# Performance work log

Hardware: AMD Instinct MI355X
Metric: run time of the kernel (lower is better)

Reference implementation:

```python
import jax, jax.numpy as jnp
import numpy as np

N, E, D = 50000, 800000, 128
CLAMP = 2.0  # coord_weights_clamp_value


def setup_inputs() -> dict:
    key = jax.random.key(0)
    ks = jax.random.split(key, 12)
    rn = lambda k, shape, scale: jax.random.normal(k, shape, jnp.float32) * scale
    s = lambda fan_in: 1.0 / np.sqrt(fan_in)
    h = rn(ks[0], (N, D), 1.0)
    x = rn(ks[1], (N, 3), 1.0)
    edges = jax.random.randint(ks[2], (2, E), 0, N)
    # edge MLP: Linear(2D+1 -> D), SiLU, Linear(D -> D), SiLU
    we1 = rn(ks[3], (2 * D + 1, D), s(2 * D + 1)); be1 = jnp.zeros((D,), jnp.float32)
    we2 = rn(ks[4], (D, D), s(D));                 be2 = jnp.zeros((D,), jnp.float32)
    # node MLP: Linear(2D -> D), SiLU, Linear(D -> D)
    wn1 = rn(ks[5], (2 * D, D), s(2 * D));         bn1 = jnp.zeros((D,), jnp.float32)
    wn2 = rn(ks[6], (D, D), s(D));                 bn2 = jnp.zeros((D,), jnp.float32)
    # coord MLP: Linear(D -> D), SiLU, Linear(D -> 1, no bias, small init)
    wc1 = rn(ks[7], (D, D), s(D));                 bc1 = jnp.zeros((D,), jnp.float32)
    wc2 = rn(ks[8], (D, 1), 0.001)
    return dict(h=h, x=x, edges=edges, we1=we1, be1=be1, we2=we2, be2=be2,
                wn1=wn1, bn1=bn1, wn2=wn2, bn2=bn2, wc1=wc1, bc1=bc1, wc2=wc2)


def reference(h, x, edges, we1, be1, we2, be2, wn1, bn1, wn2, bn2, wc1, bc1, wc2):
    n = h.shape[0]
    row, col = edges[0], edges[1]
    # coord2radial
    coord_diff = x[row] - x[col]                                  # [E, 3]
    radial = jnp.sum(coord_diff * coord_diff, axis=1, keepdims=True)  # [E, 1]
    # edge model: phi_e(h_i, h_j, ||x_i - x_j||^2)
    e_in = jnp.concatenate([h[row], h[col], radial], axis=1)      # [E, 2D+1]
    m = jax.nn.silu(jax.nn.silu(e_in @ we1 + be1) @ we2 + be2)    # [E, D]
    # coord model: x_i += mean_j (x_i - x_j) * phi_x(m_ij), clamped
    w = jax.nn.silu(m @ wc1 + bc1) @ wc2                          # [E, 1]
    trans = jnp.clip(coord_diff * w, -CLAMP, CLAMP)               # [E, 3]
    ones = jnp.ones((row.shape[0], 1), m.dtype)
    cnt = jax.ops.segment_sum(ones, row, num_segments=n)          # [N, 1]
    agg_x = jax.ops.segment_sum(trans, row, num_segments=n) / jnp.maximum(cnt, 1.0)
    x_out = x + agg_x
    # node model: h_i += phi_h(h_i, sum_j m_ij)  (residual=True)
    agg_m = jax.ops.segment_sum(m, row, num_segments=n)           # [N, D]
    h_up = jax.nn.silu(jnp.concatenate([h, agg_m], axis=1) @ wn1 + bn1) @ wn2 + bn2
    h_out = h + h_up
    return (h_out, x_out)
```

## Files before the change

### kernel.cpp

```cpp
#include <hip/hip_runtime.h>
#include <hip/hip_bf16.h>
#include <stdint.h>

typedef unsigned short u16;
typedef __bf16 bf16x8 __attribute__((ext_vector_type(8)));
typedef float f32x4 __attribute__((ext_vector_type(4)));

#define DD 128

__device__ __forceinline__ u16 f2bf(float f) {
  uint32_t r;
  asm("v_cvt_pk_bf16_f32 %0, %1, %2" : "=v"(r) : "v"(f), "v"(f));
  return (u16)r;
}
__device__ __forceinline__ float bf2f(u16 h) {
  union { uint32_t u; float f; } v; v.u = ((uint32_t)h) << 16;
  return v.f;
}
__device__ __forceinline__ uint32_t pack2(float a, float b) {
  uint32_t r;
  asm("v_cvt_pk_bf16_f32 %0, %1, %2" : "=v"(r) : "v"(a), "v"(b));
  return r;
}
__device__ __forceinline__ float silu_(float v) {
  return v * __builtin_amdgcn_rcpf(1.0f + __expf(-v));
}
__device__ __forceinline__ f32x4 MFMA(bf16x8 a, bf16x8 b, f32x4 c) {
  return __builtin_amdgcn_mfma_f32_16x16x32_bf16(a, b, c, 0, 0, 0);
}
#define LGKM_FENCE() do { asm volatile("s_waitcnt lgkmcnt(0)" ::: "memory"); __builtin_amdgcn_sched_barrier(0); } while (0)

__global__ __launch_bounds__(256) void kprep(
    const float* __restrict__ we1, const float* __restrict__ we2,
    const float* __restrict__ wn1, const float* __restrict__ wn2,
    const float* __restrict__ wc1, u16* __restrict__ frags) {
  const int total = 16384 * 5 + 32768;
  for (int idx = blockIdx.x * blockDim.x + threadIdx.x; idx < total;
       idx += gridDim.x * blockDim.x) {
    const float* src; int segbase;
    if (idx < 16384)      { src = we1;          segbase = 0; }
    else if (idx < 32768) { src = we1 + 16384;  segbase = 16384; }
    else if (idx < 49152) { src = we2;          segbase = 32768; }
    else if (idx < 65536) { src = wc1;          segbase = 49152; }
    else if (idx < 81920) { src = wn2;          segbase = 65536; }
    else                  { src = wn1;          segbase = 81920; }
    int local = idx - segbase;
    int k = local >> 7, n = local & 127;
    float v = src[k * 128 + n];
    int s = k >> 5, i = k & 7, g = (k >> 3) & 3;
    int lane = (g << 4) | (n & 15), f = n >> 4;
    frags[segbase + (((s * 8 + f) * 64 + lane) << 3) + i] = f2bf(v);
  }
}

__global__ __launch_bounds__(256) void kpq(
    const float* __restrict__ h, const float* __restrict__ be1,
    const u16* __restrict__ wA, const u16* __restrict__ wB,
    u16* __restrict__ Pb, u16* __restrict__ Qb, int N) {
  __shared__ u16 act[64 * 128];
  const int tid = threadIdx.x;
  const int w = tid >> 6, l = tid & 63;
  const int lm = l & 15, lh = l >> 4;
  const int base = blockIdx.x * 64;

  {
    const int q = l & 3;
    const int rowL = w * 16 + (l >> 2);
    int node = base + rowL; if (node >= N) node = N - 1;
    const float* hs = h + (size_t)node * 128 + q * 32;
    #pragma unroll
    for (int c4 = 0; c4 < 4; ++c4) {
      float4 v0 = *(const float4*)(hs + c4 * 8);
      float4 v1 = *(const float4*)(hs + c4 * 8 + 4);
      uint4 pk;
      pk.x = pack2(v0.x, v0.y); pk.y = pack2(v0.z, v0.w);
      pk.z = pack2(v1.x, v1.y); pk.w = pack2(v1.z, v1.w);
      int c = q * 4 + c4;
      *(uint4*)&act[rowL * 128 + (((c ^ (rowL & 7))) << 3)] = pk;
    }
  }
  LGKM_FENCE();
  const int rowA = w * 16 + lm, sw = rowA & 7;
  bf16x8 a[4];
  #pragma unroll
  for (int s = 0; s < 4; ++s)
    a[s] = *(const bf16x8*)&act[rowA * 128 + (((4 * s + lh) ^ sw) << 3)];
  float be1r[8];
  #pragma unroll
  for (int f = 0; f < 8; ++f) be1r[f] = be1[16 * f + lm];

  f32x4 acc[8] = {};
  #pragma unroll
  for (int s = 0; s < 4; ++s)
    #pragma unroll
    for (int f = 0; f < 8; ++f)
      acc[f] = MFMA(a[s], *(const bf16x8*)(wA + (((s * 8 + f) * 64 + l) << 3)), acc[f]);
  #pragma unroll
  for (int f = 0; f < 8; ++f)
    #pragma unroll
    for (int r = 0; r < 4; ++r) {
      int row = base + w * 16 + lh * 4 + r;
      Pb[(size_t)row * 128 + 16 * f + lm] = f2bf(acc[f][r] + be1r[f]);
    }

  f32x4 acc2[8] = {};
  #pragma unroll
  for (int s = 0; s < 4; ++s)
    #pragma unroll
    for (int f = 0; f < 8; ++f)
      acc2[f] = MFMA(a[s], *(const bf16x8*)(wB + (((s * 8 + f) * 64 + l) << 3)), acc2[f]);
  #pragma unroll
  for (int f = 0; f < 8; ++f)
    #pragma unroll
    for (int r = 0; r < 4; ++r) {
      int row = base + w * 16 + lh * 4 + r;
      Qb[(size_t)row * 128 + 16 * f + lm] = f2bf(acc2[f][r]);
    }
}


__global__ __launch_bounds__(256) void kedgeA(
    const float* __restrict__ x, const int* __restrict__ edges,
    const float* __restrict__ we1, const float* __restrict__ be2,
    const float* __restrict__ bc1, const float* __restrict__ wc2,
    const u16* __restrict__ Pb, const u16* __restrict__ Qb,
    const u16* __restrict__ we2f, const u16* __restrict__ wc1f,
    u16* __restrict__ mT, float* __restrict__ trans4, int E) {
  __shared__ u16 act[64 * 128];
  __shared__ float w1c[128];
  const int tid = threadIdx.x;
  if (tid < 128) w1c[tid] = we1[256 * 128 + tid];
  __syncthreads();

  const int w = tid >> 6, l = tid & 63;
  const int lm = l & 15, lh = l >> 4;
  float be2r[8], bc1r[8], wc2r[8];
  #pragma unroll
  for (int f = 0; f < 8; ++f) {
    be2r[f] = be2[16 * f + lm];
    bc1r[f] = bc1[16 * f + lm];
    wc2r[f] = wc2[16 * f + lm];
  }

  const int tb = blockIdx.x * 64 + w * 16;
  int eMine = tb + lm;
  int eC = eMine < E ? eMine : E - 1;
  const int rowv = edges[eC];
  const int colv = edges[E + eC];
  float cdx = x[rowv * 3]     - x[colv * 3];
  float cdy = x[rowv * 3 + 1] - x[colv * 3 + 1];
  float cdz = x[rowv * 3 + 2] - x[colv * 3 + 2];
  float radial = cdx * cdx + cdy * cdy + cdz * cdz;

  {
    const int el = l >> 2, q = l & 3;
    int rG = __shfl(rowv, el), cG = __shfl(colv, el);
    float rad = __shfl(radial, el);
    const int rowL = w * 16 + el;
    const u16* Pp = Pb + (size_t)rG * 128 + q * 32;
    const u16* Qp = Qb + (size_t)cG * 128 + q * 32;
    #pragma unroll
    for (int c4 = 0; c4 < 4; ++c4) {
      uint4 pv = *(const uint4*)(Pp + c4 * 8);
      uint4 qv = *(const uint4*)(Qp + c4 * 8);
      uint32_t pw[4] = {pv.x, pv.y, pv.z, pv.w};
      uint32_t qw[4] = {qv.x, qv.y, qv.z, qv.w};
      uint32_t ow[4];
      #pragma unroll
      for (int jj = 0; jj < 4; ++jj) {
        int fb = q * 32 + c4 * 8 + jj * 2;
        float t0 = bf2f((u16)(pw[jj] & 0xffff)) + bf2f((u16)(qw[jj] & 0xffff)) + rad * w1c[fb];
        float t1 = bf2f((u16)(pw[jj] >> 16))    + bf2f((u16)(qw[jj] >> 16))    + rad * w1c[fb + 1];
        ow[jj] = pack2(silu_(t0), silu_(t1));
      }
      int c = q * 4 + c4;
      *(uint4*)&act[rowL * 128 + ((c ^ (rowL & 7)) << 3)] =
          make_uint4(ow[0], ow[1], ow[2], ow[3]);
    }
  }
  LGKM_FENCE();

  const int rowA = w * 16 + lm, sw = rowA & 7;
  bf16x8 a[4];
  #pragma unroll
  for (int s = 0; s < 4; ++s)
    a[s] = *(const bf16x8*)&act[rowA * 128 + (((4 * s + lh) ^ sw) << 3)];

  f32x4 acc[8] = {};
  #pragma unroll
  for (int s = 0; s < 4; ++s)
    #pragma unroll
    for (int f = 0; f < 8; ++f)
      acc[f] = MFMA(a[s], *(const bf16x8*)(we2f + (((s * 8 + f) * 64 + l) << 3)), acc[f]);

  bool ev[4];
  #pragma unroll
  for (int r = 0; r < 4; ++r) ev[r] = (tb + lh * 4 + r) < E;
  u16* mTb = mT + (size_t)(blockIdx.x * 4 + w) * 2048;

  #pragma unroll
  for (int f = 0; f < 8; ++f)
    #pragma unroll
    for (int r = 0; r < 4; ++r) {
      float m = silu_(acc[f][r] + be2r[f]);
      u16 mv = f2bf(m);
      int row = w * 16 + lh * 4 + r, col = 16 * f + lm;
      act[row * 128 + (((col >> 3) ^ (row & 7)) << 3) + (col & 7)] = mv;
      if (ev[r]) mTb[((lh * 4 + r) * 16 + lm) * 8 + f] = mv;
    }
  LGKM_FENCE();

  bf16x8 a2[4];
  #pragma unroll
  for (int s = 0; s < 4; ++s)
    a2[s] = *(const bf16x8*)&act[rowA * 128 + (((4 * s + lh) ^ sw) << 3)];
  f32x4 acc3[8] = {};
  #pragma unroll
  for (int s = 0; s < 4; ++s)
    #pragma unroll
    for (int f = 0; f < 8; ++f)
      acc3[f] = MFMA(a2[s], *(const bf16x8*)(wc1f + (((s * 8 + f) * 64 + l) << 3)), acc3[f]);

  float wp[4] = {0.f, 0.f, 0.f, 0.f};
  #pragma unroll
  for (int f = 0; f < 8; ++f)
    #pragma unroll
    for (int r = 0; r < 4; ++r)
      wp[r] += silu_(acc3[f][r] + bc1r[f]) * wc2r[f];
  #pragma unroll
  for (int r = 0; r < 4; ++r) {
    wp[r] += __shfl_xor(wp[r], 1);
    wp[r] += __shfl_xor(wp[r], 2);
    wp[r] += __shfl_xor(wp[r], 4);
    wp[r] += __shfl_xor(wp[r], 8);
  }
  #pragma unroll
  for (int r = 0; r < 4; ++r) {
    int erv = __shfl(rowv, lh * 4 + r);
    float cdxr = __shfl(cdx, lh * 4 + r);
    float cdyr = __shfl(cdy, lh * 4 + r);
    float cdzr = __shfl(cdz, lh * 4 + r);
    if (lm < 4 && ev[r]) {
      float wv = wp[r];
      float v3;
      if (lm == 0)      v3 = fminf(fmaxf(cdxr * wv, -2.0f), 2.0f);
      else if (lm == 1) v3 = fminf(fmaxf(cdyr * wv, -2.0f), 2.0f);
      else if (lm == 2) v3 = fminf(fmaxf(cdzr * wv, -2.0f), 2.0f);
      else              v3 = __int_as_float(erv);
      trans4[(size_t)(tb + lh * 4 + r) * 4 + lm] = v3;
    }
  }
}

__global__ __launch_bounds__(256) void kscat(
    const u16* __restrict__ mT, const float* __restrict__ trans4,
    float* __restrict__ aggm, float* __restrict__ aggx, int E) {
  const int tid = threadIdx.x;
  const int w = tid >> 6, l = tid & 63;
  const int lh = l >> 4, lm = l & 15;
  const int tile = blockIdx.x * 4 + w;
  const int tb = tile * 16;

  const u16* base = mT + (size_t)tile * 2048;
  bf16x8 ch[4];
  #pragma unroll
  for (int r = 0; r < 4; ++r)
    ch[r] = *(const bf16x8*)(base + ((lh * 4 + r) * 16 + lm) * 8);

  int eL = tb + (l >> 2);
  float tv = (eL < E) ? trans4[(size_t)eL * 4 + (l & 3)] : __int_as_float(-1);

  int erOwn = __float_as_int(__shfl(tv, (l >> 2) * 4 + 3));
  if (erOwn >= 0) {
    float val = ((l & 3) == 3) ? 1.0f : tv;
    unsafeAtomicAdd(&aggx[(size_t)erOwn * 4 + (l & 3)], val);
  }

  #pragma unroll
  for (int r = 0; r < 4; ++r) {
    int er = __float_as_int(__shfl(tv, (lh * 4 + r) * 4 + 3));
    if (er >= 0) {
      const u16* hp = (const u16*)&ch[r];
      #pragma unroll
      for (int f = 0; f < 8; ++f)
        unsafeAtomicAdd(&aggm[(size_t)er * 128 + 16 * f + lm], bf2f(hp[f]));
    }
  }
}

__global__ __launch_bounds__(256) void kedge_mono(
    const float* __restrict__ x, const int* __restrict__ edges,
    const float* __restrict__ we1, const float* __restrict__ be2,
    const float* __restrict__ bc1, const float* __restrict__ wc2,
    const u16* __restrict__ Pb, const u16* __restrict__ Qb,
    const u16* __restrict__ we2f, const u16* __restrict__ wc1f,
    float* __restrict__ aggm, float* __restrict__ aggx, int E) {
  __shared__ u16 act[64 * 128];
  __shared__ float w1c[128];
  const int tid = threadIdx.x;
  if (tid < 128) w1c[tid] = we1[256 * 128 + tid];
  __syncthreads();

  const int w = tid >> 6, l = tid & 63;
  const int lm = l & 15, lh = l >> 4;
  float be2r[8], bc1r[8], wc2r[8];
  #pragma unroll
  for (int f = 0; f < 8; ++f) {
    be2r[f] = be2[16 * f + lm];
    bc1r[f] = bc1[16 * f + lm];
    wc2r[f] = wc2[16 * f + lm];
  }

  const int tb = blockIdx.x * 64 + w * 16;
  int eMine = tb + lm;
  int eC = eMine < E ? eMine : E - 1;
  const int rowv = edges[eC];
  const int colv = edges[E + eC];
  float cdx = x[rowv * 3]     - x[colv * 3];
  float cdy = x[rowv * 3 + 1] - x[colv * 3 + 1];
  float cdz = x[rowv * 3 + 2] - x[colv * 3 + 2];
  float radial = cdx * cdx + cdy * cdy + cdz * cdz;

  {
    const int el = l >> 2, q = l & 3;
    int rG = __shfl(rowv, el), cG = __shfl(colv, el);
    float rad = __shfl(radial, el);
    const int rowL = w * 16 + el;
    const u16* Pp = Pb + (size_t)rG * 128 + q * 32;
    const u16* Qp = Qb + (size_t)cG * 128 + q * 32;
    #pragma unroll
    for (int c4 = 0; c4 < 4; ++c4) {
      uint4 pv = *(const uint4*)(Pp + c4 * 8);
      uint4 qv = *(const uint4*)(Qp + c4 * 8);
      uint32_t pw[4] = {pv.x, pv.y, pv.z, pv.w};
      uint32_t qw[4] = {qv.x, qv.y, qv.z, qv.w};
      uint32_t ow[4];
      #pragma unroll
      for (int jj = 0; jj < 4; ++jj) {
        int fb = q * 32 + c4 * 8 + jj * 2;
        float t0 = bf2f((u16)(pw[jj] & 0xffff)) + bf2f((u16)(qw[jj] & 0xffff)) + rad * w1c[fb];
        float t1 = bf2f((u16)(pw[jj] >> 16))    + bf2f((u16)(qw[jj] >> 16))    + rad * w1c[fb + 1];
        ow[jj] = pack2(silu_(t0), silu_(t1));
      }
      int c = q * 4 + c4;
      *(uint4*)&act[rowL * 128 + ((c ^ (rowL & 7)) << 3)] =
          make_uint4(ow[0], ow[1], ow[2], ow[3]);
    }
  }
  LGKM_FENCE();

  const int rowA = w * 16 + lm, sw = rowA & 7;
  bf16x8 a[4];
  #pragma unroll
  for (int s = 0; s < 4; ++s)
    a[s] = *(const bf16x8*)&act[rowA * 128 + (((4 * s + lh) ^ sw) << 3)];

  f32x4 acc[8] = {};
  #pragma unroll
  for (int s = 0; s < 4; ++s)
    #pragma unroll
    for (int f = 0; f < 8; ++f)
      acc[f] = MFMA(a[s], *(const bf16x8*)(we2f + (((s * 8 + f) * 64 + l) << 3)), acc[f]);

  #pragma unroll
  for (int f = 0; f < 8; ++f)
    #pragma unroll
    for (int r = 0; r < 4; ++r) {
      float m = silu_(acc[f][r] + be2r[f]);
      int row = w * 16 + lh * 4 + r, col = 16 * f + lm;
      act[row * 128 + (((col >> 3) ^ (row & 7)) << 3) + (col & 7)] = f2bf(m);
    }
  LGKM_FENCE();

  bf16x8 a2[4];
  #pragma unroll
  for (int s = 0; s < 4; ++s)
    a2[s] = *(const bf16x8*)&act[rowA * 128 + (((4 * s + lh) ^ sw) << 3)];
  f32x4 acc3[8] = {};
  #pragma unroll
  for (int s = 0; s < 4; ++s)
    #pragma unroll
    for (int f = 0; f < 8; ++f)
      acc3[f] = MFMA(a2[s], *(const bf16x8*)(wc1f + (((s * 8 + f) * 64 + l) << 3)), acc3[f]);

  float wp[4] = {0.f, 0.f, 0.f, 0.f};
  #pragma unroll
  for (int f = 0; f < 8; ++f)
    #pragma unroll
    for (int r = 0; r < 4; ++r)
      wp[r] += silu_(acc3[f][r] + bc1r[f]) * wc2r[f];
  #pragma unroll
  for (int r = 0; r < 4; ++r) {
    wp[r] += __shfl_xor(wp[r], 1);
    wp[r] += __shfl_xor(wp[r], 2);
    wp[r] += __shfl_xor(wp[r], 4);
    wp[r] += __shfl_xor(wp[r], 8);
  }
  int er[4]; bool vr[4];
  float cdxr[4], cdyr[4], cdzr[4];
  #pragma unroll
  for (int r = 0; r < 4; ++r) {
    er[r] = __shfl(rowv, lh * 4 + r);
    vr[r] = (tb + lh * 4 + r) < E;
    cdxr[r] = __shfl(cdx, lh * 4 + r);
    cdyr[r] = __shfl(cdy, lh * 4 + r);
    cdzr[r] = __shfl(cdz, lh * 4 + r);
  }

  if (lm < 4) {
    #pragma unroll
    for (int r = 0; r < 4; ++r) {
      if (vr[r]) {
        float wv = wp[r];
        float v3;
        if (lm == 0)      v3 = fminf(fmaxf(cdxr[r] * wv, -2.0f), 2.0f);
        else if (lm == 1) v3 = fminf(fmaxf(cdyr[r] * wv, -2.0f), 2.0f);
        else if (lm == 2) v3 = fminf(fmaxf(cdzr[r] * wv, -2.0f), 2.0f);
        else              v3 = 1.0f;
        unsafeAtomicAdd(&aggx[(size_t)er[r] * 4 + lm], v3);
      }
    }
  }
  #pragma unroll
  for (int f = 0; f < 8; ++f)
    #pragma unroll
    for (int r = 0; r < 4; ++r) {
      if (vr[r]) {
        float m = silu_(acc[f][r] + be2r[f]);
        unsafeAtomicAdd(&aggm[(size_t)er[r] * 128 + 16 * f + lm], m);
      }
    }
}

__global__ __launch_bounds__(256) void knode(
    const float* __restrict__ h, const float* __restrict__ x,
    const float* __restrict__ aggm, const float* __restrict__ aggx,
    const float* __restrict__ bn1, const float* __restrict__ bn2,
    const u16* __restrict__ wn1f, const u16* __restrict__ wn2f,
    float* __restrict__ out, int N) {
  __shared__ u16 act[64 * 256];
  __shared__ u16 act2[64 * 128];
  const int tid = threadIdx.x;
  const int w = tid >> 6, l = tid & 63;
  const int lm = l & 15, lh = l >> 4;
  const int base = blockIdx.x * 64;

  if (tid < 192) {
    int n = base + tid / 3, c = tid - (tid / 3) * 3;
    if (n < N) {
      float ct = fmaxf(aggx[(size_t)n * 4 + 3], 1.0f);
      out[(size_t)N * 128 + (size_t)n * 3 + c] =
          x[(size_t)n * 3 + c] + aggx[(size_t)n * 4 + c] / ct;
    }
  }

  {
    const int q = l & 3;
    const int rowL = w * 16 + (l >> 2);
    int node = base + rowL; if (node >= N) node = N - 1;
    const float* src = (q < 2) ? (h + (size_t)node * 128 + q * 64)
                               : (aggm + (size_t)node * 128 + (q - 2) * 64);
    #pragma unroll
    for (int c8 = 0; c8 < 8; ++c8) {
      float4 v0 = *(const float4*)(src + c8 * 8);
      float4 v1 = *(const float4*)(src + c8 * 8 + 4);
      uint4 pk;
      pk.x = pack2(v0.x, v0.y); pk.y = pack2(v0.z, v0.w);
      pk.z = pack2(v1.x, v1.y); pk.w = pack2(v1.z, v1.w);
      int c = q * 8 + c8;
      *(uint4*)&act[rowL * 256 + ((c ^ (rowL & 7)) << 3)] = pk;
    }
  }
  LGKM_FENCE();

  const int rowA = w * 16 + lm, sw = rowA & 7;
  float bn1r[8], bn2r[8];
  #pragma unroll
  for (int f = 0; f < 8; ++f) {
    bn1r[f] = bn1[16 * f + lm];
    bn2r[f] = bn2[16 * f + lm];
  }
  bf16x8 a[8];
  #pragma unroll
  for (int s = 0; s < 8; ++s)
    a[s] = *(const bf16x8*)&act[rowA * 256 + (((4 * s + lh) ^ sw) << 3)];
  f32x4 acc[8] = {};
  #pragma unroll
  for (int s = 0; s < 8; ++s)
    #pragma unroll
    for (int f = 0; f < 8; ++f)
      acc[f] = MFMA(a[s], *(const bf16x8*)(wn1f + (((s * 8 + f) * 64 + l) << 3)), acc[f]);
  #pragma unroll
  for (int f = 0; f < 8; ++f)
    #pragma unroll
    for (int r = 0; r < 4; ++r) {
      int row = w * 16 + lh * 4 + r, col = 16 * f + lm;
      act2[row * 128 + (((col >> 3) ^ (row & 7)) << 3) + (col & 7)] =
          f2bf(silu_(acc[f][r] + bn1r[f]));
    }
  LGKM_FENCE();

  bf16x8 a2[4];
  #pragma unroll
  for (int s = 0; s < 4; ++s)
    a2[s] = *(const bf16x8*)&act2[rowA * 128 + (((4 * s + lh) ^ sw) << 3)];
  f32x4 acc2[8] = {};
  #pragma unroll
  for (int s = 0; s < 4; ++s)
    #pragma unroll
    for (int f = 0; f < 8; ++f)
      acc2[f] = MFMA(a2[s], *(const bf16x8*)(wn2f + (((s * 8 + f) * 64 + l) << 3)), acc2[f]);
  #pragma unroll
  for (int f = 0; f < 8; ++f)
    #pragma unroll
    for (int r = 0; r < 4; ++r) {
      int n2 = base + w * 16 + lh * 4 + r;
      if (n2 < N) {
        int col = 16 * f + lm;
        out[(size_t)n2 * 128 + col] =
            h[(size_t)n2 * 128 + col] + acc2[f][r] + bn2r[f];
      }
    }
}

extern "C" void kernel_launch(void* const* d_in, const int* in_sizes, int n_in,
                              void* d_out, int out_size, void* d_ws, size_t ws_size,
                              hipStream_t stream) {
  const float* h   = (const float*)d_in[0];
  const float* x   = (const float*)d_in[1];
  const int* edges = (const int*)d_in[2];
  const float* we1 = (const float*)d_in[3];
  const float* be1 = (const float*)d_in[4];
  const float* we2 = (const float*)d_in[5];
  const float* be2 = (const float*)d_in[6];
  const float* wn1 = (const float*)d_in[7];
  const float* bn1 = (const float*)d_in[8];
  const float* wn2 = (const float*)d_in[9];
  const float* bn2 = (const float*)d_in[10];
  const float* wc1 = (const float*)d_in[11];
  const float* bc1 = (const float*)d_in[12];
  const float* wc2 = (const float*)d_in[13];

  const int N = in_sizes[0] / DD;
  const int E = in_sizes[2] / 2;
  const int NT = (N + 63) & ~63;
  const int ET = (E + 15) & ~15;

  u16* Pb    = (u16*)d_ws;
  u16* Qb    = Pb + (size_t)NT * DD;
  u16* frags = Qb + (size_t)NT * DD;
  float* aggm = (float*)(frags + 114688);
  float* aggx = aggm + (size_t)NT * DD;
  u16* mT     = (u16*)(aggx + (size_t)NT * 4);
  float* trans4 = (float*)(mT + (size_t)ET * DD);

  size_t need_small = (size_t)NT * DD * 2 * 2 + 114688 * 2 +
                      (size_t)NT * (DD * 4 + 16);
  size_t need_big = need_small + (size_t)ET * DD * 2 + (size_t)ET * 16;
  if (ws_size < need_small) return;

  hipMemsetAsync(aggm, 0, (size_t)NT * (DD * 4 + 16), stream);
  hipLaunchKernelGGL(kprep, dim3(64), dim3(256), 0, stream,
                     we1, we2, wn1, wn2, wc1, frags);
  hipLaunchKernelGGL(kpq, dim3(NT / 64), dim3(256), 0, stream,
                     h, be1, frags, frags + 16384, Pb, Qb, N);
  if (ws_size >= need_big) {
    hipLaunchKernelGGL(kedgeA, dim3((E + 63) / 64), dim3(256), 0, stream,
                       x, edges, we1, be2, bc1, wc2, Pb, Qb,
                       frags + 32768, frags + 49152, mT, trans4, E);
    hipLaunchKernelGGL(kscat, dim3((ET / 16 + 3) / 4), dim3(256), 0, stream,
                       mT, trans4, aggm, aggx, E);
  } else {
    hipLaunchKernelGGL(kedge_mono, dim3((E + 63) / 64), dim3(256), 0, stream,
                       x, edges, we1, be2, bc1, wc2, Pb, Qb,
                       frags + 32768, frags + 49152, aggm, aggx, E);
  }
  hipLaunchKernelGGL(knode, dim3(NT / 64), dim3(256), 0, stream,
                     h, x, aggm, aggx, bn1, bn2,
                     frags + 81920, frags + 65536, (float*)d_out, N);
}
```

Baseline: 453.9 us.

## Fuse edge MLP with scatter atomics and prefetch next tile's P/Q gathers

Replaces the two-kernel edge path (edge MLP writing m and trans to a buffer, then a separate scatter kernel) with one kernel that does the atomics for agg_m and agg_x directly. Each wave now handles four 16-edge tiles and prefetches the next tile's P/Q rows while the current tile runs its MFMAs. Coordinate differences and radial are precomputed by a small kernel and stored as bf16. This removes the round trip of the m buffer through global memory but cuts coordinate precision to bf16, and it raises register pressure from the prefetch buffers.

```diff
diff --git a/kernel.cpp b/kernel.cpp
--- a/kernel.cpp
+++ b/kernel.cpp
@@ -5,6 +5,7 @@
 typedef unsigned short u16;
 typedef __bf16 bf16x8 __attribute__((ext_vector_type(8)));
 typedef float f32x4 __attribute__((ext_vector_type(4)));
+typedef unsigned int u32x4 __attribute__((ext_vector_type(4)));
 
 #define DD 128
 
@@ -53,6 +54,19 @@
   }
 }
 
+__global__ __launch_bounds__(256) void kradial(
+    const int* __restrict__ edges, const float* __restrict__ x,
+    uint2* __restrict__ cdr, int E) {
+  int i = blockIdx.x * 256 + threadIdx.x;
+  if (i >= E) return;
+  int r = edges[i], c = edges[E + i];
+  float dx = x[r * 3]     - x[c * 3];
+  float dy = x[r * 3 + 1] - x[c * 3 + 1];
+  float dz = x[r * 3 + 2] - x[c * 3 + 2];
+  float rad = dx * dx + dy * dy + dz * dz;
+  cdr[i] = make_uint2(pack2(dx, dy), pack2(dz, rad));
+}
+
 __global__ __launch_bounds__(256) void kpq(
     const float* __restrict__ h, const float* __restrict__ be1,
     const u16* __restrict__ wA, const u16* __restrict__ wB,
@@ -118,14 +132,13 @@
     }
 }
 
-
-__global__ __launch_bounds__(256) void kedgeA(
-    const float* __restrict__ x, const int* __restrict__ edges,
+__global__ __launch_bounds__(256) void kedgeP(
+    const int* __restrict__ edges, const uint2* __restrict__ cdr,
     const float* __restrict__ we1, const float* __restrict__ be2,
     const float* __restrict__ bc1, const float* __restrict__ wc2,
     const u16* __restrict__ Pb, const u16* __restrict__ Qb,
     const u16* __restrict__ we2f, const u16* __restrict__ wc1f,
-    u16* __restrict__ mT, float* __restrict__ trans4, int E) {
+    float* __restrict__ aggm, float* __restrict__ aggx, int E) {
   __shared__ u16 act[64 * 128];
   __shared__ float w1c[128];
   const int tid = threadIdx.x;
@@ -134,6 +147,7 @@
 
   const int w = tid >> 6, l = tid & 63;
   const int lm = l & 15, lh = l >> 4;
+  const int el = l >> 2, q = l & 3;
   float be2r[8], bc1r[8], wc2r[8];
   #pragma unroll
   for (int f = 0; f < 8; ++f) {
@@ -142,148 +156,161 @@
     wc2r[f] = wc2[16 * f + lm];
   }
 
-  const int tb = blockIdx.x * 64 + w * 16;
-  int eMine = tb + lm;
-  int eC = eMine < E ? eMine : E - 1;
-  const int rowv = edges[eC];
-  const int colv = edges[E + eC];
-  float cdx = x[rowv * 3]     - x[colv * 3];
-  float cdy = x[rowv * 3 + 1] - x[colv * 3 + 1];
-  float cdz = x[rowv * 3 + 2] - x[colv * 3 + 2];
-  float radial = cdx * cdx + cdy * cdy + cdz * cdz;
-
+  const int tb = blockIdx.x * 256 + w * 64;
+  const int rowA = w * 16 + lm, sw = rowA & 7;
+  const int rowL = w * 16 + el;
+
+  int rv[4], cv[4]; uint2 cdu[4];
+  #pragma unroll
+  for (int t = 0; t < 4; ++t) {
+    int e = tb + t * 16 + lm;
+    int ec = e < E ? e : E - 1;
+    rv[t] = edges[ec];
+    cv[t] = edges[E + ec];
+    cdu[t] = cdr[ec];
+  }
+
+  u32x4 Pc[4], Qc[4], Pn[4], Qn[4];
   {
-    const int el = l >> 2, q = l & 3;
-    int rG = __shfl(rowv, el), cG = __shfl(colv, el);
-    float rad = __shfl(radial, el);
-    const int rowL = w * 16 + el;
+    int rG = __shfl(rv[0], el), cG = __shfl(cv[0], el);
     const u16* Pp = Pb + (size_t)rG * 128 + q * 32;
     const u16* Qp = Qb + (size_t)cG * 128 + q * 32;
     #pragma unroll
     for (int c4 = 0; c4 < 4; ++c4) {
-      uint4 pv = *(const uint4*)(Pp + c4 * 8);
-      uint4 qv = *(const uint4*)(Qp + c4 * 8);
-      uint32_t pw[4] = {pv.x, pv.y, pv.z, pv.w};
-      uint32_t qw[4] = {qv.x, qv.y, qv.z, qv.w};
-      uint32_t ow[4];
-      #pragma unroll
-      for (int jj = 0; jj < 4; ++jj) {
-        int fb = q * 32 + c4 * 8 + jj * 2;
-        float t0 = bf2f((u16)(pw[jj] & 0xffff)) + bf2f((u16)(qw[jj] & 0xffff)) + rad * w1c[fb];
-        float t1 = bf2f((u16)(pw[jj] >> 16))    + bf2f((u16)(qw[jj] >> 16))    + rad * w1c[fb + 1];
-        ow[jj] = pack2(silu_(t0), silu_(t1));
-      }
-      int c = q * 4 + c4;
-      *(uint4*)&act[rowL * 128 + ((c ^ (rowL & 7)) << 3)] =
-          make_uint4(ow[0], ow[1], ow[2], ow[3]);
-    }
-  }
-  LGKM_FENCE();
-
-  const int rowA = w * 16 + lm, sw = rowA & 7;
-  bf16x8 a[4];
-  #pragma unroll
-  for (int s = 0; s < 4; ++s)
-    a[s] = *(const bf16x8*)&act[rowA * 128 + (((4 * s + lh) ^ sw) << 3)];
-
-  f32x4 acc[8] = {};
-  #pragma unroll
-  for (int s = 0; s < 4; ++s)
-    #pragma unroll
-    for (int f = 0; f < 8; ++f)
-      acc[f] = MFMA(a[s], *(const bf16x8*)(we2f + (((s * 8 + f) * 64 + l) << 3)), acc[f]);
-
-  bool ev[4];
-  #pragma unroll
-  for (int r = 0; r < 4; ++r) ev[r] = (tb + lh * 4 + r) < E;
-  u16* mTb = mT + (size_t)(blockIdx.x * 4 + w) * 2048;
-
-  #pragma unroll
-  for (int f = 0; f < 8; ++f)
-    #pragma unroll
-    for (int r = 0; r < 4; ++r) {
-      float m = silu_(acc[f][r] + be2r[f]);
-      u16 mv = f2bf(m);
-      int row = w * 16 + lh * 4 + r, col = 16 * f + lm;
-      act[row * 128 + (((col >> 3) ^ (row & 7)) << 3) + (col & 7)] = mv;
-      if (ev[r]) mTb[((lh * 4 + r) * 16 + lm) * 8 + f] = mv;
-    }
-  LGKM_FENCE();
-
-  bf16x8 a2[4];
-  #pragma unroll
-  for (int s = 0; s < 4; ++s)
-    a2[s] = *(const bf16x8*)&act[rowA * 128 + (((4 * s + lh) ^ sw) << 3)];
-  f32x4 acc3[8] = {};
-  #pragma unroll
-  for (int s = 0; s < 4; ++s)
-    #pragma unroll
-    for (int f = 0; f < 8; ++f)
-      acc3[f] = MFMA(a2[s], *(const bf16x8*)(wc1f + (((s * 8 + f) * 64 + l) << 3)), acc3[f]);
-
-  float wp[4] = {0.f, 0.f, 0.f, 0.f};
-  #pragma unroll
-  for (int f = 0; f < 8; ++f)
-    #pragma unroll
-    for (int r = 0; r < 4; ++r)
-      wp[r] += silu_(acc3[f][r] + bc1r[f]) * wc2r[f];
-  #pragma unroll
-  for (int r = 0; r < 4; ++r) {
-    wp[r] += __shfl_xor(wp[r], 1);
-    wp[r] += __shfl_xor(wp[r], 2);
-    wp[r] += __shfl_xor(wp[r], 4);
-    wp[r] += __shfl_xor(wp[r], 8);
-  }
-  #pragma unroll
-  for (int r = 0; r < 4; ++r) {
-    int erv = __shfl(rowv, lh * 4 + r);
-    float cdxr = __shfl(cdx, lh * 4 + r);
-    float cdyr = __shfl(cdy, lh * 4 + r);
-    float cdzr = __shfl(cdz, lh * 4 + r);
-    if (lm < 4 && ev[r]) {
-      float wv = wp[r];
-      float v3;
-      if (lm == 0)      v3 = fminf(fmaxf(cdxr * wv, -2.0f), 2.0f);
-      else if (lm == 1) v3 = fminf(fmaxf(cdyr * wv, -2.0f), 2.0f);
-      else if (lm == 2) v3 = fminf(fmaxf(cdzr * wv, -2.0f), 2.0f);
-      else              v3 = __int_as_float(erv);
-      trans4[(size_t)(tb + lh * 4 + r) * 4 + lm] = v3;
-    }
-  }
-}
-
-__global__ __launch_bounds__(256) void kscat(
-    const u16* __restrict__ mT, const float* __restrict__ trans4,
-    float* __restrict__ aggm, float* __restrict__ aggx, int E) {
-  const int tid = threadIdx.x;
-  const int w = tid >> 6, l = tid & 63;
-  const int lh = l >> 4, lm = l & 15;
-  const int tile = blockIdx.x * 4 + w;
-  const int tb = tile * 16;
-
-  const u16* base = mT + (size_t)tile * 2048;
-  bf16x8 ch[4];
-  #pragma unroll
-  for (int r = 0; r < 4; ++r)
-    ch[r] = *(const bf16x8*)(base + ((lh * 4 + r) * 16 + lm) * 8);
-
-  int eL = tb + (l >> 2);
-  float tv = (eL < E) ? trans4[(size_t)eL * 4 + (l & 3)] : __int_as_float(-1);
-
-  int erOwn = __float_as_int(__shfl(tv, (l >> 2) * 4 + 3));
-  if (erOwn >= 0) {
-    float val = ((l & 3) == 3) ? 1.0f : tv;
-    unsafeAtomicAdd(&aggx[(size_t)erOwn * 4 + (l & 3)], val);
-  }
-
-  #pragma unroll
-  for (int r = 0; r < 4; ++r) {
-    int er = __float_as_int(__shfl(tv, (lh * 4 + r) * 4 + 3));
-    if (er >= 0) {
-      const u16* hp = (const u16*)&ch[r];
+      Pc[c4] = *(const u32x4*)(Pp + c4 * 8);
+      Qc[c4] = *(const u32x4*)(Qp + c4 * 8);
+    }
+  }
+
+  #pragma unroll
+  for (int t = 0; t < 4; ++t) {
+    {
+      float radf = bf2f((u16)(cdu[t].y >> 16));
+      float rad = __shfl(radf, el);
+      #pragma unroll
+      for (int c4 = 0; c4 < 4; ++c4) {
+        uint32_t pw[4] = {Pc[c4].x, Pc[c4].y, Pc[c4].z, Pc[c4].w};
+        uint32_t qw[4] = {Qc[c4].x, Qc[c4].y, Qc[c4].z, Qc[c4].w};
+        uint32_t ow[4];
+        #pragma unroll
+        for (int jj = 0; jj < 4; ++jj) {
+          int fb = q * 32 + c4 * 8 + jj * 2;
+          float t0 = bf2f((u16)(pw[jj] & 0xffff)) + bf2f((u16)(qw[jj] & 0xffff)) + rad * w1c[fb];
+          float t1 = bf2f((u16)(pw[jj] >> 16))    + bf2f((u16)(qw[jj] >> 16))    + rad * w1c[fb + 1];
+          ow[jj] = pack2(silu_(t0), silu_(t1));
+        }
+        int c = q * 4 + c4;
+        *(uint4*)&act[rowL * 128 + ((c ^ (rowL & 7)) << 3)] =
+            make_uint4(ow[0], ow[1], ow[2], ow[3]);
+      }
+    }
+    LGKM_FENCE();
+
+    bf16x8 a[4];
+    #pragma unroll
+    for (int s = 0; s < 4; ++s)
+      a[s] = *(const bf16x8*)&act[rowA * 128 + (((4 * s + lh) ^ sw) << 3)];
+
+    if (t < 3) {
+      int rG = __shfl(rv[t + 1], el), cG = __shfl(cv[t + 1], el);
+      const u16* Pp = Pb + (size_t)rG * 128 + q * 32;
+      const u16* Qp = Qb + (size_t)cG * 128 + q * 32;
+      #pragma unroll
+      for (int c4 = 0; c4 < 4; ++c4) {
+        Pn[c4] = *(const u32x4*)(Pp + c4 * 8);
+        Qn[c4] = *(const u32x4*)(Qp + c4 * 8);
+      }
+    }
+
+    f32x4 acc[8] = {};
+    #pragma unroll
+    for (int s = 0; s < 4; ++s)
       #pragma unroll
       for (int f = 0; f < 8; ++f)
-        unsafeAtomicAdd(&aggm[(size_t)er * 128 + 16 * f + lm], bf2f(hp[f]));
+        acc[f] = MFMA(a[s], *(const bf16x8*)(we2f + (((s * 8 + f) * 64 + l) << 3)), acc[f]);
+
+    uint32_t pk_m[8][2];
+    #pragma unroll
+    for (int f = 0; f < 8; ++f) {
+      float mv[4];
+      #pragma unroll
+      for (int r = 0; r < 4; ++r) {
+        mv[r] = silu_(acc[f][r] + be2r[f]);
+        int row = w * 16 + lh * 4 + r, col = 16 * f + lm;
+        act[row * 128 + (((col >> 3) ^ (row & 7)) << 3) + (col & 7)] = f2bf(mv[r]);
+      }
+      pk_m[f][0] = pack2(mv[0], mv[1]);
+      pk_m[f][1] = pack2(mv[2], mv[3]);
+    }
+    LGKM_FENCE();
+
+    bf16x8 a2[4];
+    #pragma unroll
+    for (int s = 0; s < 4; ++s)
+      a2[s] = *(const bf16x8*)&act[rowA * 128 + (((4 * s + lh) ^ sw) << 3)];
+    f32x4 acc3[8] = {};
+    #pragma unroll
+    for (int s = 0; s < 4; ++s)
+      #pragma unroll
+      for (int f = 0; f < 8; ++f)
+        acc3[f] = MFMA(a2[s], *(const bf16x8*)(wc1f + (((s * 8 + f) * 64 + l) << 3)), acc3[f]);
+
+    float wp[4] = {0.f, 0.f, 0.f, 0.f};
+    #pragma unroll
+    for (int f = 0; f < 8; ++f)
+      #pragma unroll
+      for (int r = 0; r < 4; ++r)
+        wp[r] += silu_(acc3[f][r] + bc1r[f]) * wc2r[f];
+    #pragma unroll
+    for (int r = 0; r < 4; ++r) {
+      wp[r] += __shfl_xor(wp[r], 1);
+      wp[r] += __shfl_xor(wp[r], 2);
+      wp[r] += __shfl_xor(wp[r], 4);
+      wp[r] += __shfl_xor(wp[r], 8);
+    }
+
+    float cdx = bf2f((u16)(cdu[t].x & 0xffff));
+    float cdy = bf2f((u16)(cdu[t].x >> 16));
+    float cdz = bf2f((u16)(cdu[t].y & 0xffff));
+    int er[4]; bool vr[4];
+    float cdxr[4], cdyr[4], cdzr[4];
+    #pragma unroll
+    for (int r = 0; r < 4; ++r) {
+      er[r] = __shfl(rv[t], lh * 4 + r);
+      vr[r] = (tb + t * 16 + lh * 4 + r) < E;
+      cdxr[r] = __shfl(cdx, lh * 4 + r);
+      cdyr[r] = __shfl(cdy, lh * 4 + r);
+      cdzr[r] = __shfl(cdz, lh * 4 + r);
+    }
+
+    if (lm < 4) {
+      #pragma unroll
+      for (int r = 0; r < 4; ++r) {
+        if (vr[r]) {
+          float wv = wp[r];
+          float v3;
+          if (lm == 0)      v3 = fminf(fmaxf(cdxr[r] * wv, -2.0f), 2.0f);
+          else if (lm == 1) v3 = fminf(fmaxf(cdyr[r] * wv, -2.0f), 2.0f);
+          else if (lm == 2) v3 = fminf(fmaxf(cdzr[r] * wv, -2.0f), 2.0f);
+          else              v3 = 1.0f;
+          unsafeAtomicAdd(&aggx[(size_t)er[r] * 4 + lm], v3);
+        }
+      }
+    }
+
+    #pragma unroll
+    for (int f = 0; f < 8; ++f)
+      #pragma unroll
+      for (int r = 0; r < 4; ++r) {
+        if (vr[r]) {
+          float m = bf2f((u16)((pk_m[f][r >> 1] >> ((r & 1) * 16)) & 0xffff));
+          unsafeAtomicAdd(&aggm[(size_t)er[r] * 128 + 16 * f + lm], m);
+        }
+      }
+
+    if (t < 3) {
+      #pragma unroll
+      for (int c4 = 0; c4 < 4; ++c4) { Pc[c4] = Pn[c4]; Qc[c4] = Qn[c4]; }
     }
   }
 }
@@ -336,11 +363,11 @@
       uint32_t qw[4] = {qv.x, qv.y, qv.z, qv.w};
       uint32_t ow[4];
       #pragma unroll
-      for (int jj = 0; jj < 4; ++jj) {
-        int fb = q * 32 + c4 * 8 + jj * 2;
-        float t0 = bf2f((u16)(pw[jj] & 0xffff)) + bf2f((u16)(qw[jj] & 0xffff)) + rad * w1c[fb];
-        float t1 = bf2f((u16)(pw[jj] >> 16))    + bf2f((u16)(qw[jj] >> 16))    + rad * w1c[fb + 1];
-        ow[jj] = pack2(silu_(t0), silu_(t1));
+      for (int t2 = 0; t2 < 4; ++t2) {
+        int fb = q * 32 + c4 * 8 + t2 * 2;
+        float t0 = bf2f((u16)(pw[t2] & 0xffff)) + bf2f((u16)(qw[t2] & 0xffff)) + rad * w1c[fb];
+        float t1 = bf2f((u16)(pw[t2] >> 16))    + bf2f((u16)(qw[t2] >> 16))    + rad * w1c[fb + 1];
+        ow[t2] = pack2(silu_(t0), silu_(t1));
       }
       int c = q * 4 + c4;
       *(uint4*)&act[rowL * 128 + ((c ^ (rowL & 7)) << 3)] =
@@ -544,32 +571,31 @@
   const int N = in_sizes[0] / DD;
   const int E = in_sizes[2] / 2;
   const int NT = (N + 63) & ~63;
-  const int ET = (E + 15) & ~15;
 
   u16* Pb    = (u16*)d_ws;
   u16* Qb    = Pb + (size_t)NT * DD;
   u16* frags = Qb + (size_t)NT * DD;
   float* aggm = (float*)(frags + 114688);
   float* aggx = aggm + (size_t)NT * DD;
-  u16* mT     = (u16*)(aggx + (size_t)NT * 4);
-  float* trans4 = (float*)(mT + (size_t)ET * DD);
-
-  size_t need_small = (size_t)NT * DD * 2 * 2 + 114688 * 2 +
-                      (size_t)NT * (DD * 4 + 16);
-  size_t need_big = need_small + (size_t)ET * DD * 2 + (size_t)ET * 16;
-  if (ws_size < need_small) return;
-
-  hipMemsetAsync(aggm, 0, (size_t)NT * (DD * 4 + 16), stream);
+  uint2* cdr = (uint2*)(aggx + (size_t)NT * 4);
+
+  size_t need_mono = (size_t)NT * DD * 2 * 2 + 114688 * 2 +
+                     (size_t)NT * (DD * 4 + 16);
+  size_t need_pipe = need_mono + (size_t)E * 8;
+  if (ws_size < need_mono) return;
+
   hipLaunchKernelGGL(kprep, dim3(64), dim3(256), 0, stream,
                      we1, we2, wn1, wn2, wc1, frags);
   hipLaunchKernelGGL(kpq, dim3(NT / 64), dim3(256), 0, stream,
                      h, be1, frags, frags + 16384, Pb, Qb, N);
-  if (ws_size >= need_big) {
-    hipLaunchKernelGGL(kedgeA, dim3((E + 63) / 64), dim3(256), 0, stream,
-                       x, edges, we1, be2, bc1, wc2, Pb, Qb,
-                       frags + 32768, frags + 49152, mT, trans4, E);
-    hipLaunchKernelGGL(kscat, dim3((ET / 16 + 3) / 4), dim3(256), 0, stream,
-                       mT, trans4, aggm, aggx, E);
+  hipMemsetAsync(aggm, 0, (size_t)NT * (DD * 4 + 16), stream);
+
+  if (ws_size >= need_pipe) {
+    hipLaunchKernelGGL(kradial, dim3((E + 255) / 256), dim3(256), 0, stream,
+                       edges, x, cdr, E);
+    hipLaunchKernelGGL(kedgeP, dim3((E + 255) / 256), dim3(256), 0, stream,
+                       edges, cdr, we1, be2, bc1, wc2, Pb, Qb,
+                       frags + 32768, frags + 49152, aggm, aggx, E);
   } else {
     hipLaunchKernelGGL(kedge_mono, dim3((E + 63) / 64), dim3(256), 0, stream,
                        x, edges, we1, be2, bc1, wc2, Pb, Qb,
```

Result: slower. 551.1 us (+21.4%).
